# Kernel optimization log

Measured on AMD Instinct MI355X. Metric: run time of the kernel, lower is better.

## Reference

```python
import jax, jax.numpy as jnp
import numpy as np

B, C, H, W = 16, 320, 32, 32
DK, DV, NH = 640, 64, 4   # dk = k*planes = 2*320, dv = int(0.2*320)
CO = C - DV               # conv_out channels = planes - dv = 256
EPS = 1e-5


def _conv(x, w, b, pad):
    out = jax.lax.conv_general_dilated(x, w, (1, 1), [(pad, pad), (pad, pad)],
                                       dimension_numbers=('NCHW', 'OIHW', 'NCHW'))
    return out + b[None, :, None, None]


def _bn_relu(x, g, b, m, v):
    scale = (g * jax.lax.rsqrt(v + EPS))[None, :, None, None]
    y = (x - m[None, :, None, None]) * scale + b[None, :, None, None]
    return jax.nn.relu(y)


def _rel_to_abs(x):
    # x: (B, N, L, 2L-1) -> (B, N, L, L)
    b, n, L, _ = x.shape
    x = jnp.pad(x, ((0, 0), (0, 0), (0, 0), (0, 1)))          # (B,N,L,2L)
    flat = x.reshape(b, n, L * 2 * L)
    flat = jnp.pad(flat, ((0, 0), (0, 0), (0, L - 1)))
    return flat.reshape(b, n, L + 1, 2 * L - 1)[:, :, :L, L - 1:]


def _relative_logits_1d(q, rel_k, case):
    # q: (B, Nh, Hq, Wq, dkh)
    b, nh, hq, wq, _ = q.shape
    rel = jnp.einsum('bnxyd,md->bnxym', q, rel_k)              # (B,Nh,Hq,Wq,2Wq-1)
    rel = _rel_to_abs(rel.reshape(b, nh * hq, wq, 2 * wq - 1))  # (B,Nh*Hq,Wq,Wq)
    rel = jnp.broadcast_to(rel.reshape(b, nh, hq, 1, wq, wq), (b, nh, hq, hq, wq, wq))
    if case == 'w':
        rel = rel.transpose(0, 1, 2, 4, 3, 5)
    else:  # 'h'
        rel = rel.transpose(0, 1, 4, 2, 5, 3)
    return rel.reshape(b, nh, hq * wq, hq * wq)


def _aug_conv(x, conv_w, conv_b, qkv_w, qkv_b, attn_w, attn_b, rel_w, rel_h):
    conv_out = _conv(x, conv_w, conv_b, 1)                     # (B,CO,H,W)
    qkv = _conv(x, qkv_w, qkv_b, 1)                            # (B,2*DK+DV,H,W)
    b = x.shape[0]
    q, k, v = jnp.split(qkv, [DK, 2 * DK], axis=1)
    dkh, dvh = DK // NH, DV // NH
    q = q.reshape(b, NH, dkh, H, W) * (dkh ** -0.5)
    k = k.reshape(b, NH, dkh, H * W)
    v = v.reshape(b, NH, dvh, H * W)
    logits = jnp.einsum('bndp,bndq->bnpq', q.reshape(b, NH, dkh, H * W), k)
    q_bhwd = q.transpose(0, 1, 3, 4, 2)                        # (B,Nh,H,W,dkh)
    logits = logits + _relative_logits_1d(q_bhwd, rel_w, 'w')
    logits = logits + _relative_logits_1d(q_bhwd.transpose(0, 1, 3, 2, 4), rel_h, 'h')
    wts = jax.nn.softmax(logits, axis=-1)                      # (B,Nh,HW,HW)
    attn = jnp.einsum('bnpq,bndq->bnpd', wts, v)               # (B,Nh,HW,dvh)
    # NOTE: raw reshape (not a transpose), faithful to the original repo's code
    attn = attn.reshape(b, DV, H, W)
    attn = _conv(attn, attn_w, attn_b, 0)
    return jnp.concatenate([conv_out, attn], axis=1)           # (B,C,H,W)


def setup_inputs() -> dict:
    key = jax.random.key(0)
    ks = iter(jax.random.split(key, 48))
    def nrm(shape, s=1.0):
        return jax.random.normal(next(ks), shape, jnp.float32) * s
    d = {"x": nrm((B, C, H, W))}
    for p in ("bn1", "bn2"):
        d[p + "_g"] = jax.random.uniform(next(ks), (C,), jnp.float32, 0.5, 1.5)
        d[p + "_b"] = nrm((C,), 0.1)
        d[p + "_m"] = nrm((C,), 0.1)
        d[p + "_v"] = jax.random.uniform(next(ks), (C,), jnp.float32, 0.5, 1.5)
    s3 = 1.0 / np.sqrt(C * 9)
    for p in ("c1", "c2"):
        d[p + "_conv_w"] = nrm((CO, C, 3, 3), s3)
        d[p + "_conv_b"] = nrm((CO,), 0.01)
        d[p + "_qkv_w"] = nrm((2 * DK + DV, C, 3, 3), s3)
        d[p + "_qkv_b"] = nrm((2 * DK + DV,), 0.01)
        d[p + "_attn_w"] = nrm((DV, DV, 1, 1), 1.0 / np.sqrt(DV))
        d[p + "_attn_b"] = nrm((DV,), 0.01)
        d[p + "_rel_w"] = nrm((2 * W - 1, DK // NH), 0.1)
        d[p + "_rel_h"] = nrm((2 * H - 1, DK // NH), 0.1)
    return d


def reference(x, bn1_g, bn1_b, bn1_m, bn1_v,
              c1_conv_w, c1_conv_b, c1_qkv_w, c1_qkv_b, c1_attn_w, c1_attn_b, c1_rel_w, c1_rel_h,
              bn2_g, bn2_b, bn2_m, bn2_v,
              c2_conv_w, c2_conv_b, c2_qkv_w, c2_qkv_b, c2_attn_w, c2_attn_b, c2_rel_w, c2_rel_h):
    out = _aug_conv(_bn_relu(x, bn1_g, bn1_b, bn1_m, bn1_v),
                    c1_conv_w, c1_conv_b, c1_qkv_w, c1_qkv_b,
                    c1_attn_w, c1_attn_b, c1_rel_w, c1_rel_h)
    # dropout is identity in eval mode (and dropout_rate=0)
    out = _aug_conv(_bn_relu(out, bn2_g, bn2_b, bn2_m, bn2_v),
                    c2_conv_w, c2_conv_b, c2_qkv_w, c2_qkv_b,
                    c2_attn_w, c2_attn_b, c2_rel_w, c2_rel_h)
    return out + x  # identity shortcut (stride=1, in_planes==planes)
```

## Files before the change

### kernel.cpp

```cpp
#include <hip/hip_runtime.h>
#include <hip/hip_bf16.h>

#define B_   16
#define C_   320
#define HW_  1024
#define CO_  256
#define NH_  4
#define DKH_ 160
#define QKVC 1344
#define FCO  1600

using bf16x8 = __attribute__((ext_vector_type(8))) __bf16;
using f32x4  = __attribute__((ext_vector_type(4))) float;

static __device__ __forceinline__ bf16x8 bzero8() {
  bf16x8 r;
#pragma unroll
  for (int j = 0; j < 8; ++j) r[j] = (__bf16)0.0f;
  return r;
}

__global__ void transform_all(const float* __restrict__ wc, const float* __restrict__ wq,
                              __bf16* __restrict__ wt,
                              const float* __restrict__ rw, const float* __restrict__ rh,
                              __bf16* __restrict__ rwb, __bf16* __restrict__ rhb) {
  int idx = blockIdx.x * 256 + threadIdx.x;
  if (idx < FCO * C_) {
    int ci = idx % C_;
    int co = idx / C_;
    const float* src = (co < CO_) ? (wc + ((size_t)co * C_ + ci) * 9)
                                  : (wq + ((size_t)(co - CO_) * C_ + ci) * 9);
#pragma unroll
    for (int t = 0; t < 9; ++t)
      wt[((size_t)t * FCO + co) * C_ + ci] = (__bf16)src[t];
  } else {
    int r = idx - FCO * C_;
    if (r < 63 * DKH_) {
      rwb[r] = (__bf16)rw[r];
      rhb[r] = (__bf16)rh[r];
    }
  }
}

template <typename TI>
__global__ __launch_bounds__(256)
void bn_relu_t(const TI* __restrict__ x, const float* __restrict__ g,
               const float* __restrict__ bb, const float* __restrict__ m,
               const float* __restrict__ v, __bf16* __restrict__ y) {
  __shared__ __bf16 tile[32][33];
  int b = blockIdx.z, c0 = blockIdx.y * 32, p0 = blockIdx.x * 32;
#pragma unroll
  for (int i = 0; i < 4; ++i) {
    int cl = threadIdx.y + i * 8;
    int c = c0 + cl;
    int p = p0 + threadIdx.x;
    float scale = g[c] * rsqrtf(v[c] + 1e-5f);
    float val = ((float)x[((size_t)b * C_ + c) * HW_ + p] - m[c]) * scale + bb[c];
    tile[cl][threadIdx.x] = (__bf16)fmaxf(val, 0.0f);
  }
  __syncthreads();
#pragma unroll
  for (int i = 0; i < 4; ++i) {
    int pl = threadIdx.y + i * 8;
    int p = p0 + pl;
    int c = c0 + threadIdx.x;
    y[((size_t)b * HW_ + p) * C_ + c] = tile[threadIdx.x][pl];
  }
}

template <typename TO>
__global__ __launch_bounds__(256, 3)
void conv3x3_fused(const __bf16* __restrict__ y, const __bf16* __restrict__ wt,
                   const float* __restrict__ bias_c, const float* __restrict__ bias_q,
                   TO* __restrict__ out, const float* __restrict__ resid,
                   __bf16* __restrict__ qt, __bf16* __restrict__ kt,
                   __bf16* __restrict__ vt) {
  __shared__ __align__(16) char act_s[204 * 128];
  __shared__ __align__(16) char w_s[128 * 128];

  int tid = threadIdx.x;
  int lane = tid & 63, wv = tid >> 6;
  int lr = lane & 15, lg = lane >> 4;

  int hw_lin = blockIdx.x + 8 * blockIdx.y + 104 * blockIdx.z;
  int xcd = hw_lin & 7, seq = hw_lin >> 3;
  int yhat = seq >> 4;
  int pair = (seq & 15) * 8 + xcd;
  int xhat = pair & 7, zhat = pair >> 3;

  int b = zhat;
  int co_blk = yhat * 128;
  int h0 = xhat * 4;
  int wco = wv >> 1, wp = wv & 1;

  f32x4 zz = {0.f, 0.f, 0.f, 0.f};
  f32x4 acc[4][4];
#pragma unroll
  for (int m = 0; m < 4; ++m)
#pragma unroll
    for (int n = 0; n < 4; ++n) acc[m][n] = zz;

  int rbase[4], cbase[4];
#pragma unroll
  for (int n = 0; n < 4; ++n) {
    int pb = wp * 64 + n * 16 + lr;
    rbase[n] = (pb >> 5) + 1;
    cbase[n] = (pb & 31) + 1;
  }

  const __bf16* ybase = y + (size_t)b * HW_ * C_;

  int rl8 = lane >> 3;
  int k8 = lane & 7;
  int swoff = (k8 ^ rl8) * 8;
  const __bf16* wsrc[4];
#pragma unroll
  for (int i = 0; i < 4; ++i) {
    int co = co_blk + i * 32 + wv * 8 + rl8;
    if (co > FCO - 1) co = FCO - 1;
    wsrc[i] = wt + (size_t)co * C_ + swoff;
  }

  auto stage_W = [&](int tap, int chunk) {
    size_t woff = (size_t)tap * FCO * C_ + chunk * 64;
#pragma unroll
    for (int i = 0; i < 4; ++i)
      __builtin_amdgcn_global_load_lds(
          (const __attribute__((address_space(1))) void*)(wsrc[i] + woff),
          (__attribute__((address_space(3))) void*)(w_s + i * 4096 + wv * 1024),
          16, 0, 0);
  };
  auto stage_act = [&](int chunk) {
    int ci0 = chunk * 64;
    for (int g = tid; g < 1632; g += 256) {
      int gi = g & 7, slot = g >> 3;
      int row = slot / 34, col = slot - row * 34;
      int h = h0 + row - 1, c = col - 1;
      bf16x8 val;
      if ((unsigned)h < 32u && (unsigned)c < 32u)
        val = *(const bf16x8*)(ybase + ((size_t)(h * 32 + c)) * C_ + ci0 + gi * 8);
      else
        val = bzero8();
      *(bf16x8*)(act_s + ((slot * 128 + gi * 16) ^ ((col & 7) << 4))) = val;
    }
  };

  stage_act(0);
  stage_W(0, 0);

  for (int cb = 0; cb < 5; ++cb) {
    for (int tap = 0; tap < 9; ++tap) {
      __syncthreads();
      bf16x8 af[2][4];
#pragma unroll
      for (int ks = 0; ks < 2; ++ks)
#pragma unroll
        for (int m = 0; m < 4; ++m) {
          int co_l = wco * 64 + m * 16 + lr;
          af[ks][m] = *(const bf16x8*)(w_s + ((co_l * 128 + ks * 64 + lg * 16) ^ ((co_l & 7) << 4)));
        }
      __syncthreads();
      if (!(cb == 4 && tap == 8))
        stage_W(tap == 8 ? 0 : tap + 1, tap == 8 ? cb + 1 : cb);
      int dh = tap / 3 - 1, dw = tap % 3 - 1;
#pragma unroll
      for (int ks = 0; ks < 2; ++ks) {
        bf16x8 bfv[4];
#pragma unroll
        for (int n = 0; n < 4; ++n) {
          int row = rbase[n] + dh, col = cbase[n] + dw;
          bfv[n] = *(const bf16x8*)(act_s + (((row * 34 + col) * 128 + ks * 64 + lg * 16) ^ ((col & 7) << 4)));
        }
#pragma unroll
        for (int m = 0; m < 4; ++m)
#pragma unroll
          for (int n = 0; n < 4; ++n)
            acc[m][n] = __builtin_amdgcn_mfma_f32_16x16x32_bf16(af[ks][m], bfv[n], acc[m][n], 0, 0, 0);
      }
      if (tap == 8 && cb < 4) {
        __syncthreads();
        stage_act(cb + 1);
      }
    }
  }

  const float scaleq = 0.07905694150420949f;
  int p_blk = xhat * 128;
#pragma unroll
  for (int m = 0; m < 4; ++m) {
#pragma unroll
    for (int n = 0; n < 4; ++n) {
#pragma unroll
      for (int r = 0; r < 4; ++r) {
        int co = co_blk + wco * 64 + m * 16 + lg * 4 + r;
        if (co >= FCO) continue;
        int p = p_blk + wp * 64 + n * 16 + lr;
        if (co < CO_) {
          float val = acc[m][n][r] + bias_c[co];
          size_t o = ((size_t)b * C_ + co) * HW_ + p;
          if (resid) val += resid[o];
          out[o] = (TO)val;
        } else {
          int qco = co - CO_;
          float val = acc[m][n][r] + bias_q[qco];
          if (qco < 640) {
            int nn = qco / DKH_, d = qco % DKH_;
            qt[(((size_t)b * NH_ + nn) * HW_ + p) * DKH_ + d] = (__bf16)(val * scaleq);
          } else if (qco < 1280) {
            int c2 = qco - 640;
            int nn = c2 / DKH_, d = c2 % DKH_;
            kt[(((size_t)b * NH_ + nn) * HW_ + p) * DKH_ + d] = (__bf16)val;
          } else {
            int c3 = qco - 1280;
            vt[((size_t)b * 64 + c3) * HW_ + p] = (__bf16)val;
          }
        }
      }
    }
  }
}

__global__ __launch_bounds__(256, 4)
void attn_kernel(const __bf16* __restrict__ qt, const __bf16* __restrict__ kt,
                 const __bf16* __restrict__ vt, const __bf16* __restrict__ relwb,
                 const __bf16* __restrict__ relhb, __bf16* __restrict__ attn_out) {
  __shared__ float Rw_lds[16][66];
  __shared__ float Rh_lds[16][66];
  __shared__ __align__(16) __bf16 p_lds[4][16][136];
  __shared__ float smax[16][4];
  __shared__ float ssum[16][4];
  __shared__ float part[4][16][16];

  int tid = threadIdx.x;
  int lane = tid & 63, wv = tid >> 6;
  int lr = lane & 15, lg = lane >> 4;

  int hw_lin = blockIdx.x + 64 * blockIdx.y + 256 * blockIdx.z;
  int xcd = hw_lin & 7, s = hw_lin >> 3;
  int qb = s & 63;
  int g = (s >> 6) * 8 + xcd;
  int n = g & 3, b = g >> 2;

  int p0 = qb * 16;
  const size_t qkbase = ((size_t)(b * NH_ + n)) * HW_ * DKH_;

  bf16x8 qf[5];
#pragma unroll
  for (int ks = 0; ks < 5; ++ks)
    qf[ks] = *(const bf16x8*)(qt + qkbase + (size_t)(p0 + lr) * DKH_ + ks * 32 + lg * 8);

  f32x4 zz = {0.f, 0.f, 0.f, 0.f};

  {
    int relpos = wv * 16 + lr;
    bool ok = relpos < 63;
    int rp = ok ? relpos : 0;
    f32x4 accw = zz, acch = zz;
#pragma unroll
    for (int ks = 0; ks < 5; ++ks) {
      bf16x8 bw = *(const bf16x8*)(relwb + (size_t)rp * DKH_ + ks * 32 + lg * 8);
      bf16x8 bh = *(const bf16x8*)(relhb + (size_t)rp * DKH_ + ks * 32 + lg * 8);
      if (!ok) { bw = bzero8(); bh = bzero8(); }
      accw = __builtin_amdgcn_mfma_f32_16x16x32_bf16(qf[ks], bw, accw, 0, 0, 0);
      acch = __builtin_amdgcn_mfma_f32_16x16x32_bf16(qf[ks], bh, acch, 0, 0, 0);
    }
#pragma unroll
    for (int r = 0; r < 4; ++r) {
      Rw_lds[lg * 4 + r][wv * 16 + lr] = accw[r];
      Rh_lds[lg * 4 + r][wv * 16 + lr] = acch[r];
    }
  }
  __syncthreads();

  f32x4 acc[16];
#pragma unroll
  for (int t = 0; t < 16; ++t) acc[t] = zz;

  int key_base = wv * 256;
  __builtin_amdgcn_s_setprio(1);
#pragma unroll
  for (int t = 0; t < 16; ++t) {
    const __bf16* kp = kt + qkbase + (size_t)(key_base + t * 16 + lr) * DKH_ + lg * 8;
#pragma unroll
    for (int ks = 0; ks < 5; ++ks) {
      bf16x8 kf = *(const bf16x8*)(kp + ks * 32);
      acc[t] = __builtin_amdgcn_mfma_f32_16x16x32_bf16(qf[ks], kf, acc[t], 0, 0, 0);
    }
  }
  __builtin_amdgcn_s_setprio(0);

#pragma unroll
  for (int t = 0; t < 16; ++t) {
    int key = key_base + t * 16 + lr;
    int ky = key & 31, kx = key >> 5;
#pragma unroll
    for (int r = 0; r < 4; ++r) {
      int i = lg * 4 + r;
      int yi = (p0 + i) & 31, xi = (p0 + i) >> 5;
      acc[t][r] += Rw_lds[i][ky - yi + 31] + Rh_lds[i][kx - xi + 31];
    }
  }

  float mx[4];
#pragma unroll
  for (int r = 0; r < 4; ++r) {
    float m = acc[0][r];
#pragma unroll
    for (int t = 1; t < 16; ++t) m = fmaxf(m, acc[t][r]);
#pragma unroll
    for (int msk = 1; msk < 16; msk <<= 1)
      m = fmaxf(m, __shfl_xor(m, msk, 64));
    mx[r] = m;
  }
  if (lr == 0) {
#pragma unroll
    for (int r = 0; r < 4; ++r) smax[lg * 4 + r][wv] = mx[r];
  }

  const __bf16* vbase = vt + ((size_t)b * 64 + n * 16 + lr) * HW_ + key_base + lg * 8;
  float sm[4] = {0.f, 0.f, 0.f, 0.f};
  f32x4 pv_acc = zz;
#pragma unroll
  for (int half = 0; half < 2; ++half) {
    bf16x8 vfh[4];
#pragma unroll
    for (int ks = 0; ks < 4; ++ks)
      vfh[ks] = *(const bf16x8*)(vbase + (half * 4 + ks) * 32);
#pragma unroll
    for (int t = half * 8; t < half * 8 + 8; ++t) {
#pragma unroll
      for (int r = 0; r < 4; ++r) {
        float pv = __expf(acc[t][r] - mx[r]);
        __bf16 pb = (__bf16)pv;
        sm[r] += (float)pb;
        p_lds[wv][lg * 4 + r][(t & 7) * 16 + lr] = pb;
      }
    }
#pragma unroll
    for (int ks = 0; ks < 4; ++ks) {
      bf16x8 pf = *(const bf16x8*)&p_lds[wv][lr][ks * 32 + lg * 8];
      pv_acc = __builtin_amdgcn_mfma_f32_16x16x32_bf16(pf, vfh[ks], pv_acc, 0, 0, 0);
    }
  }
#pragma unroll
  for (int r = 0; r < 4; ++r) {
#pragma unroll
    for (int msk = 1; msk < 16; msk <<= 1)
      sm[r] += __shfl_xor(sm[r], msk, 64);
  }
  if (lr == 0) {
#pragma unroll
    for (int r = 0; r < 4; ++r) ssum[lg * 4 + r][wv] = sm[r];
  }

#pragma unroll
  for (int r = 0; r < 4; ++r) part[wv][lg * 4 + r][lr] = pv_acc[r];
  __syncthreads();

  int i = tid >> 4, dv = tid & 15;
  float m0 = smax[i][0], m1 = smax[i][1], m2 = smax[i][2], m3 = smax[i][3];
  float M = fmaxf(fmaxf(m0, m1), fmaxf(m2, m3));
  float e0 = __expf(m0 - M), e1 = __expf(m1 - M),
        e2 = __expf(m2 - M), e3 = __expf(m3 - M);
  float S = ssum[i][0] * e0 + ssum[i][1] * e1 + ssum[i][2] * e2 + ssum[i][3] * e3;
  float val = (part[0][i][dv] * e0 + part[1][i][dv] * e1 +
               part[2][i][dv] * e2 + part[3][i][dv] * e3) / S;
  int flat = (p0 + i) * 16 + dv;
  attn_out[((size_t)b * 64 + n * 16 + (flat >> 10)) * HW_ + (flat & 1023)] = (__bf16)val;
}

template <typename TO>
__global__ __launch_bounds__(256)
void proj1x1(const __bf16* __restrict__ attn, const float* __restrict__ w,
             const float* __restrict__ bias, TO* __restrict__ out,
             const float* __restrict__ resid) {
  __shared__ float wl[16][64];
  int tid = threadIdx.x;
  int cq = blockIdx.y, b = blockIdx.z;
  int p = blockIdx.x * 256 + tid;
  for (int i = tid; i < 1024; i += 256)
    wl[i >> 6][i & 63] = w[(cq * 16 + (i >> 6)) * 64 + (i & 63)];
  __syncthreads();
  float in[64];
#pragma unroll
  for (int c = 0; c < 64; ++c) in[c] = (float)attn[((size_t)b * 64 + c) * HW_ + p];
#pragma unroll
  for (int c = 0; c < 16; ++c) {
    int gc = cq * 16 + c;
    float a = bias[gc];
#pragma unroll
    for (int cc = 0; cc < 64; ++cc) a += wl[c][cc] * in[cc];
    size_t o = ((size_t)b * C_ + 256 + gc) * HW_ + p;
    if (resid) a += resid[o];
    out[o] = (TO)a;
  }
}

extern "C" void kernel_launch(void* const* d_in, const int* in_sizes, int n_in,
                              void* d_out, int out_size, void* d_ws, size_t ws_size,
                              hipStream_t stream) {
  (void)in_sizes; (void)n_in; (void)out_size;
  const float* x = (const float*)d_in[0];
  const float* bn_g[2]   = {(const float*)d_in[1],  (const float*)d_in[5]};
  const float* bn_b[2]   = {(const float*)d_in[2],  (const float*)d_in[6]};
  const float* bn_m[2]   = {(const float*)d_in[3],  (const float*)d_in[7]};
  const float* bn_v[2]   = {(const float*)d_in[4],  (const float*)d_in[8]};
  const float* conv_w[2] = {(const float*)d_in[9],  (const float*)d_in[17]};
  const float* conv_b[2] = {(const float*)d_in[10], (const float*)d_in[18]};
  const float* qkv_w[2]  = {(const float*)d_in[11], (const float*)d_in[19]};
  const float* qkv_b[2]  = {(const float*)d_in[12], (const float*)d_in[20]};
  const float* attn_w[2] = {(const float*)d_in[13], (const float*)d_in[21]};
  const float* attn_b[2] = {(const float*)d_in[14], (const float*)d_in[22]};
  const float* rel_w[2]  = {(const float*)d_in[15], (const float*)d_in[23]};
  const float* rel_h[2]  = {(const float*)d_in[16], (const float*)d_in[24]};

  char* ws = (char*)d_ws;
  size_t off = 0;
  auto take = [&](size_t bytes) {
    char* p = ws + off;
    off += (bytes + 255) & ~(size_t)255;
    return p;
  };
  __bf16* y_nhwc = (__bf16*)take((size_t)B_ * HW_ * C_ * 2);
  __bf16* qt     = (__bf16*)take((size_t)B_ * NH_ * HW_ * DKH_ * 2);
  __bf16* kt2    = (__bf16*)take((size_t)B_ * NH_ * HW_ * DKH_ * 2);
  __bf16* vt     = (__bf16*)take((size_t)B_ * 64 * HW_ * 2);
  __bf16* attn_c = (__bf16*)take((size_t)B_ * 64 * HW_ * 2);
  __bf16* l1out  = (__bf16*)take((size_t)B_ * C_ * HW_ * 2);
  __bf16* wt_s   = (__bf16*)take((size_t)9 * FCO * C_ * 2);
  __bf16* rel_wb = (__bf16*)take((size_t)63 * DKH_ * 2);
  __bf16* rel_hb = (__bf16*)take((size_t)63 * DKH_ * 2);
  if (ws_size < off) return;

  const int ntrans = (FCO * C_ + 63 * DKH_ + 255) / 256;

  for (int l = 0; l < 2; ++l) {
    const float* resid = (l == 0) ? nullptr : x;

    if (l == 0)
      bn_relu_t<float><<<dim3(32, 10, 16), dim3(32, 8), 0, stream>>>(
          x, bn_g[l], bn_b[l], bn_m[l], bn_v[l], y_nhwc);
    else
      bn_relu_t<__bf16><<<dim3(32, 10, 16), dim3(32, 8), 0, stream>>>(
          l1out, bn_g[l], bn_b[l], bn_m[l], bn_v[l], y_nhwc);

    transform_all<<<ntrans, 256, 0, stream>>>(
        conv_w[l], qkv_w[l], wt_s, rel_w[l], rel_h[l], rel_wb, rel_hb);

    if (l == 0)
      conv3x3_fused<__bf16><<<dim3(8, 13, 16), 256, 0, stream>>>(
          y_nhwc, wt_s, conv_b[l], qkv_b[l], l1out, nullptr, qt, kt2, vt);
    else
      conv3x3_fused<float><<<dim3(8, 13, 16), 256, 0, stream>>>(
          y_nhwc, wt_s, conv_b[l], qkv_b[l], (float*)d_out, resid, qt, kt2, vt);

    attn_kernel<<<dim3(64, NH_, 16), 256, 0, stream>>>(
        qt, kt2, vt, rel_wb, rel_hb, attn_c);

    if (l == 0)
      proj1x1<__bf16><<<dim3(4, 4, 16), 256, 0, stream>>>(
          attn_c, attn_w[l], attn_b[l], l1out, nullptr);
    else
      proj1x1<float><<<dim3(4, 4, 16), 256, 0, stream>>>(
          attn_c, attn_w[l], attn_b[l], (float*)d_out, resid);
  }
}
```

Before: 638.2 us.

## Process 32 queries per attention block with 8 waves sharing K loads

Each attention block now handles two 16-query groups with 512 threads (8 waves), and every wave covers 128 keys instead of 256. Each K fragment loaded feeds two MFMAs, one per query group, which halves K global traffic per query. The cross-wave softmax merge now combines 8 partials per row, and LDS usage and register pressure per thread rise while the grid halves.

```diff
diff --git a/kernel.cpp b/kernel.cpp
--- a/kernel.cpp
+++ b/kernel.cpp
@@ -220,39 +220,42 @@
   }
 }
 
-__global__ __launch_bounds__(256, 4)
+__global__ __launch_bounds__(512, 4)
 void attn_kernel(const __bf16* __restrict__ qt, const __bf16* __restrict__ kt,
                  const __bf16* __restrict__ vt, const __bf16* __restrict__ relwb,
                  const __bf16* __restrict__ relhb, __bf16* __restrict__ attn_out) {
-  __shared__ float Rw_lds[16][66];
-  __shared__ float Rh_lds[16][66];
-  __shared__ __align__(16) __bf16 p_lds[4][16][136];
-  __shared__ float smax[16][4];
-  __shared__ float ssum[16][4];
-  __shared__ float part[4][16][16];
+  __shared__ float Rw_lds[2][16][66];
+  __shared__ float Rh_lds[2][16][66];
+  __shared__ __align__(16) __bf16 p_lds[8][16][72];
+  __shared__ float smax[2][16][8];
+  __shared__ float ssum[2][16][8];
+  __shared__ float part[8][2][16][16];
 
   int tid = threadIdx.x;
   int lane = tid & 63, wv = tid >> 6;
   int lr = lane & 15, lg = lane >> 4;
 
-  int hw_lin = blockIdx.x + 64 * blockIdx.y + 256 * blockIdx.z;
+  int hw_lin = blockIdx.x + 32 * blockIdx.y + 128 * blockIdx.z;
   int xcd = hw_lin & 7, s = hw_lin >> 3;
-  int qb = s & 63;
-  int g = (s >> 6) * 8 + xcd;
-  int n = g & 3, b = g >> 2;
-
-  int p0 = qb * 16;
+  int qb = s & 31;
+  int gg = (s >> 5) * 8 + xcd;
+  int n = gg & 3, b = gg >> 2;
+
+  int p0 = qb * 32;
   const size_t qkbase = ((size_t)(b * NH_ + n)) * HW_ * DKH_;
 
-  bf16x8 qf[5];
-#pragma unroll
-  for (int ks = 0; ks < 5; ++ks)
-    qf[ks] = *(const bf16x8*)(qt + qkbase + (size_t)(p0 + lr) * DKH_ + ks * 32 + lg * 8);
+  bf16x8 qf[2][5];
+#pragma unroll
+  for (int g = 0; g < 2; ++g)
+#pragma unroll
+    for (int ks = 0; ks < 5; ++ks)
+      qf[g][ks] = *(const bf16x8*)(qt + qkbase + (size_t)(p0 + g * 16 + lr) * DKH_ + ks * 32 + lg * 8);
 
   f32x4 zz = {0.f, 0.f, 0.f, 0.f};
 
   {
-    int relpos = wv * 16 + lr;
+    int tg = wv >> 2;
+    int relpos = (wv & 3) * 16 + lr;
     bool ok = relpos < 63;
     int rp = ok ? relpos : 0;
     f32x4 accw = zz, acch = zz;
@@ -261,111 +264,134 @@
       bf16x8 bw = *(const bf16x8*)(relwb + (size_t)rp * DKH_ + ks * 32 + lg * 8);
       bf16x8 bh = *(const bf16x8*)(relhb + (size_t)rp * DKH_ + ks * 32 + lg * 8);
       if (!ok) { bw = bzero8(); bh = bzero8(); }
-      accw = __builtin_amdgcn_mfma_f32_16x16x32_bf16(qf[ks], bw, accw, 0, 0, 0);
-      acch = __builtin_amdgcn_mfma_f32_16x16x32_bf16(qf[ks], bh, acch, 0, 0, 0);
+      accw = __builtin_amdgcn_mfma_f32_16x16x32_bf16(qf[tg][ks], bw, accw, 0, 0, 0);
+      acch = __builtin_amdgcn_mfma_f32_16x16x32_bf16(qf[tg][ks], bh, acch, 0, 0, 0);
     }
 #pragma unroll
     for (int r = 0; r < 4; ++r) {
-      Rw_lds[lg * 4 + r][wv * 16 + lr] = accw[r];
-      Rh_lds[lg * 4 + r][wv * 16 + lr] = acch[r];
+      Rw_lds[tg][lg * 4 + r][relpos] = accw[r];
+      Rh_lds[tg][lg * 4 + r][relpos] = acch[r];
     }
   }
   __syncthreads();
 
-  f32x4 acc[16];
-#pragma unroll
-  for (int t = 0; t < 16; ++t) acc[t] = zz;
-
-  int key_base = wv * 256;
+  f32x4 acc[2][8];
+#pragma unroll
+  for (int g = 0; g < 2; ++g)
+#pragma unroll
+    for (int t = 0; t < 8; ++t) acc[g][t] = zz;
+
+  int key_base = wv * 128;
   __builtin_amdgcn_s_setprio(1);
 #pragma unroll
-  for (int t = 0; t < 16; ++t) {
+  for (int t = 0; t < 8; ++t) {
     const __bf16* kp = kt + qkbase + (size_t)(key_base + t * 16 + lr) * DKH_ + lg * 8;
 #pragma unroll
     for (int ks = 0; ks < 5; ++ks) {
       bf16x8 kf = *(const bf16x8*)(kp + ks * 32);
-      acc[t] = __builtin_amdgcn_mfma_f32_16x16x32_bf16(qf[ks], kf, acc[t], 0, 0, 0);
+      acc[0][t] = __builtin_amdgcn_mfma_f32_16x16x32_bf16(qf[0][ks], kf, acc[0][t], 0, 0, 0);
+      acc[1][t] = __builtin_amdgcn_mfma_f32_16x16x32_bf16(qf[1][ks], kf, acc[1][t], 0, 0, 0);
     }
   }
   __builtin_amdgcn_s_setprio(0);
 
 #pragma unroll
-  for (int t = 0; t < 16; ++t) {
-    int key = key_base + t * 16 + lr;
-    int ky = key & 31, kx = key >> 5;
+  for (int g = 0; g < 2; ++g)
+#pragma unroll
+    for (int t = 0; t < 8; ++t) {
+      int key = key_base + t * 16 + lr;
+      int ky = key & 31, kx = key >> 5;
+#pragma unroll
+      for (int r = 0; r < 4; ++r) {
+        int i = lg * 4 + r;
+        int q = p0 + g * 16 + i;
+        int yi = q & 31, xi = q >> 5;
+        acc[g][t][r] += Rw_lds[g][i][ky - yi + 31] + Rh_lds[g][i][kx - xi + 31];
+      }
+    }
+
+  float mx[2][4];
+#pragma unroll
+  for (int g = 0; g < 2; ++g)
 #pragma unroll
     for (int r = 0; r < 4; ++r) {
-      int i = lg * 4 + r;
-      int yi = (p0 + i) & 31, xi = (p0 + i) >> 5;
-      acc[t][r] += Rw_lds[i][ky - yi + 31] + Rh_lds[i][kx - xi + 31];
-    }
-  }
-
-  float mx[4];
-#pragma unroll
-  for (int r = 0; r < 4; ++r) {
-    float m = acc[0][r];
-#pragma unroll
-    for (int t = 1; t < 16; ++t) m = fmaxf(m, acc[t][r]);
-#pragma unroll
-    for (int msk = 1; msk < 16; msk <<= 1)
-      m = fmaxf(m, __shfl_xor(m, msk, 64));
-    mx[r] = m;
-  }
+      float m = acc[g][0][r];
+#pragma unroll
+      for (int t = 1; t < 8; ++t) m = fmaxf(m, acc[g][t][r]);
+#pragma unroll
+      for (int msk = 1; msk < 16; msk <<= 1)
+        m = fmaxf(m, __shfl_xor(m, msk, 64));
+      mx[g][r] = m;
+    }
   if (lr == 0) {
 #pragma unroll
-    for (int r = 0; r < 4; ++r) smax[lg * 4 + r][wv] = mx[r];
+    for (int g = 0; g < 2; ++g)
+#pragma unroll
+      for (int r = 0; r < 4; ++r) smax[g][lg * 4 + r][wv] = mx[g][r];
   }
 
   const __bf16* vbase = vt + ((size_t)b * 64 + n * 16 + lr) * HW_ + key_base + lg * 8;
-  float sm[4] = {0.f, 0.f, 0.f, 0.f};
-  f32x4 pv_acc = zz;
+  float sm[2][4] = {{0.f, 0.f, 0.f, 0.f}, {0.f, 0.f, 0.f, 0.f}};
+  f32x4 pv[2] = {zz, zz};
 #pragma unroll
   for (int half = 0; half < 2; ++half) {
-    bf16x8 vfh[4];
-#pragma unroll
-    for (int ks = 0; ks < 4; ++ks)
-      vfh[ks] = *(const bf16x8*)(vbase + (half * 4 + ks) * 32);
-#pragma unroll
-    for (int t = half * 8; t < half * 8 + 8; ++t) {
-#pragma unroll
-      for (int r = 0; r < 4; ++r) {
-        float pv = __expf(acc[t][r] - mx[r]);
-        __bf16 pb = (__bf16)pv;
-        sm[r] += (float)pb;
-        p_lds[wv][lg * 4 + r][(t & 7) * 16 + lr] = pb;
-      }
-    }
-#pragma unroll
-    for (int ks = 0; ks < 4; ++ks) {
-      bf16x8 pf = *(const bf16x8*)&p_lds[wv][lr][ks * 32 + lg * 8];
-      pv_acc = __builtin_amdgcn_mfma_f32_16x16x32_bf16(pf, vfh[ks], pv_acc, 0, 0, 0);
-    }
-  }
-#pragma unroll
-  for (int r = 0; r < 4; ++r) {
-#pragma unroll
-    for (int msk = 1; msk < 16; msk <<= 1)
-      sm[r] += __shfl_xor(sm[r], msk, 64);
+    bf16x8 vfh[2];
+#pragma unroll
+    for (int ks = 0; ks < 2; ++ks)
+      vfh[ks] = *(const bf16x8*)(vbase + (half * 2 + ks) * 32);
+#pragma unroll
+    for (int g = 0; g < 2; ++g) {
+#pragma unroll
+      for (int t = half * 4; t < half * 4 + 4; ++t) {
+#pragma unroll
+        for (int r = 0; r < 4; ++r) {
+          float pvv = __expf(acc[g][t][r] - mx[g][r]);
+          __bf16 pb = (__bf16)pvv;
+          sm[g][r] += (float)pb;
+          p_lds[wv][lg * 4 + r][(t & 3) * 16 + lr] = pb;
+        }
+      }
+#pragma unroll
+      for (int ks = 0; ks < 2; ++ks) {
+        bf16x8 pf = *(const bf16x8*)&p_lds[wv][lr][ks * 32 + lg * 8];
+        pv[g] = __builtin_amdgcn_mfma_f32_16x16x32_bf16(pf, vfh[ks], pv[g], 0, 0, 0);
+      }
+    }
+  }
+#pragma unroll
+  for (int g = 0; g < 2; ++g) {
+#pragma unroll
+    for (int r = 0; r < 4; ++r) {
+#pragma unroll
+      for (int msk = 1; msk < 16; msk <<= 1)
+        sm[g][r] += __shfl_xor(sm[g][r], msk, 64);
+    }
   }
   if (lr == 0) {
 #pragma unroll
-    for (int r = 0; r < 4; ++r) ssum[lg * 4 + r][wv] = sm[r];
-  }
-
-#pragma unroll
-  for (int r = 0; r < 4; ++r) part[wv][lg * 4 + r][lr] = pv_acc[r];
+    for (int g = 0; g < 2; ++g)
+#pragma unroll
+      for (int r = 0; r < 4; ++r) ssum[g][lg * 4 + r][wv] = sm[g][r];
+  }
+#pragma unroll
+  for (int g = 0; g < 2; ++g)
+#pragma unroll
+    for (int r = 0; r < 4; ++r) part[wv][g][lg * 4 + r][lr] = pv[g][r];
   __syncthreads();
 
-  int i = tid >> 4, dv = tid & 15;
-  float m0 = smax[i][0], m1 = smax[i][1], m2 = smax[i][2], m3 = smax[i][3];
-  float M = fmaxf(fmaxf(m0, m1), fmaxf(m2, m3));
-  float e0 = __expf(m0 - M), e1 = __expf(m1 - M),
-        e2 = __expf(m2 - M), e3 = __expf(m3 - M);
-  float S = ssum[i][0] * e0 + ssum[i][1] * e1 + ssum[i][2] * e2 + ssum[i][3] * e3;
-  float val = (part[0][i][dv] * e0 + part[1][i][dv] * e1 +
-               part[2][i][dv] * e2 + part[3][i][dv] * e3) / S;
-  int flat = (p0 + i) * 16 + dv;
+  int g2 = tid >> 8, i = (tid >> 4) & 15, dv = tid & 15;
+  float M = smax[g2][i][0];
+#pragma unroll
+  for (int w = 1; w < 8; ++w) M = fmaxf(M, smax[g2][i][w]);
+  float S = 0.f, val = 0.f;
+#pragma unroll
+  for (int w = 0; w < 8; ++w) {
+    float e = __expf(smax[g2][i][w] - M);
+    S += ssum[g2][i][w] * e;
+    val += part[w][g2][i][dv] * e;
+  }
+  val /= S;
+  int flat = (p0 + g2 * 16 + i) * 16 + dv;
   attn_out[((size_t)b * 64 + n * 16 + (flat >> 10)) * HW_ + (flat & 1023)] = (__bf16)val;
 }
 
@@ -454,7 +480,7 @@
       conv3x3_fused<float><<<dim3(8, 13, 16), 256, 0, stream>>>(
           y_nhwc, wt_s, conv_b[l], qkv_b[l], (float*)d_out, resid, qt, kt2, vt);
 
-    attn_kernel<<<dim3(64, NH_, 16), 256, 0, stream>>>(
+    attn_kernel<<<dim3(32, NH_, 16), 512, 0, stream>>>(
         qt, kt2, vt, rel_wb, rel_hb, attn_c);
 
     if (l == 0)
```

Measured after the change: 626.6 us. Within noise of the previous version (-1.8%).
